# Kernel optimization log

Hardware: AMD Instinct MI355X
Metric: run time of the kernel (lower is better)

Reference implementation:

```python
import jax, jax.numpy as jnp
import numpy as np

PAD_IDX = 1
NEG_BIG = jnp.float32(-1e18)


def setup_inputs() -> dict:
    key = jax.random.key(0)
    ks = jax.random.split(key, 7)
    B, L, K, D, V, C = 64, 350, 8, 300, 50000, 20
    node_sets = jax.random.randint(ks[0], (B, L), 0, V, dtype=jnp.int64)
    embedded_node = jax.random.normal(ks[1], (B, L, D), dtype=jnp.float32)
    edge_weight = jax.random.uniform(ks[2], (B, L, K), dtype=jnp.float32)
    embedded_neighbor_node = jax.random.normal(ks[3], (B, L, K, D), dtype=jnp.float32)
    information_rate = jax.random.uniform(ks[4], (V, 1), dtype=jnp.float32)
    W = jax.random.normal(ks[5], (C, D), dtype=jnp.float32) * 0.05
    b = jax.random.normal(ks[6], (C,), dtype=jnp.float32) * 0.05
    return {"node_sets": node_sets, "embedded_node": embedded_node,
            "edge_weight": edge_weight,
            "embedded_neighbor_node": embedded_neighbor_node,
            "information_rate": information_rate, "W": W, "b": b}


def reference(node_sets, embedded_node, edge_weight, embedded_neighbor_node,
              information_rate, W, b):
    # weighted neighbor messages: [B,L,K,D]
    tmp = edge_weight[..., None] * embedded_neighbor_node
    # masked_fill(tmp == 0, -1e18); dropout_rate=0 -> identity
    tmp = jnp.where(tmp == 0, NEG_BIG, tmp)
    # max-pool over neighbors K -> [B,L,D]
    M = tmp.max(axis=2)
    # gather per-node information rate [B,L,1]; padding nodes forced to 1
    ir = information_rate[node_sets]
    ir = jnp.where((node_sets == PAD_IDX)[..., None], jnp.float32(1.0), ir)
    # gated combine, sum over nodes L -> [B,D]
    combined = (1.0 - ir) * M + ir * embedded_node
    s = combined.sum(axis=1)
    # linear + relu + softmax -> [B,C]
    x = jax.nn.relu(jnp.einsum('bd,cd->bc', s, W) + b)
    return jax.nn.softmax(x, axis=1)
```

## Files before the change

kernel.cpp:

```cpp
#include <hip/hip_runtime.h>
#include <math.h>

#define Bn 64
#define Ln 350
#define Kn 8
#define Dn 300
#define Cn 20
#define SPLIT 32
#define PAD_IDX 1
#define NEG_BIG (-1e18f)

__global__ __launch_bounds__(256) void mp_reduce(
    const int* __restrict__ node_sets,
    const float* __restrict__ emb_node,
    const float* __restrict__ edge_w,
    const float* __restrict__ emb_nbr,
    const float* __restrict__ info_rate,
    float* __restrict__ s_out)
{
    __shared__ __align__(16) float sAcc[4][Dn + 4];

    const int bid  = blockIdx.x;
    const int b    = bid / SPLIT;
    const int sidx = bid % SPLIT;
    const int tid  = threadIdx.x;
    const int wave = tid >> 6;
    const int lane = tid & 63;
    const bool has1 = (lane < (Dn / 4 - 64));

    float4 acc0 = make_float4(0.f, 0.f, 0.f, 0.f);
    float4 acc1 = make_float4(0.f, 0.f, 0.f, 0.f);

    for (int j = wave;; j += 4) {
        const int l = sidx + j * SPLIT;
        if (l >= Ln) break;
        const size_t row = (size_t)b * Ln + l;

        const float* ewp = edge_w + row * Kn;
        float ewv[Kn];
        #pragma unroll
        for (int k = 0; k < Kn; ++k) ewv[k] = ewp[k];

        const int node = node_sets[row];
        const float ir = (node == PAD_IDX) ? 1.0f : info_rate[node];
        const float om = 1.0f - ir;

        const float* nb = emb_nbr + row * (size_t)(Kn * Dn);
        const float* en = emb_node + row * (size_t)Dn;

        {
            float4 m = make_float4(NEG_BIG, NEG_BIG, NEG_BIG, NEG_BIG);
            #pragma unroll
            for (int k = 0; k < Kn; ++k) {
                const float4 v = *reinterpret_cast<const float4*>(nb + k * Dn + 4 * lane);
                const float w = ewv[k];
                float x0 = w * v.x, x1 = w * v.y, x2 = w * v.z, x3 = w * v.w;
                x0 = (x0 == 0.f) ? NEG_BIG : x0;
                x1 = (x1 == 0.f) ? NEG_BIG : x1;
                x2 = (x2 == 0.f) ? NEG_BIG : x2;
                x3 = (x3 == 0.f) ? NEG_BIG : x3;
                m.x = fmaxf(m.x, x0);
                m.y = fmaxf(m.y, x1);
                m.z = fmaxf(m.z, x2);
                m.w = fmaxf(m.w, x3);
            }
            const float4 e = *reinterpret_cast<const float4*>(en + 4 * lane);
            acc0.x += om * m.x + ir * e.x;
            acc0.y += om * m.y + ir * e.y;
            acc0.z += om * m.z + ir * e.z;
            acc0.w += om * m.w + ir * e.w;
        }

        if (has1) {
            const int off = 256 + 4 * lane;
            float4 m = make_float4(NEG_BIG, NEG_BIG, NEG_BIG, NEG_BIG);
            #pragma unroll
            for (int k = 0; k < Kn; ++k) {
                const float4 v = *reinterpret_cast<const float4*>(nb + k * Dn + off);
                const float w = ewv[k];
                float x0 = w * v.x, x1 = w * v.y, x2 = w * v.z, x3 = w * v.w;
                x0 = (x0 == 0.f) ? NEG_BIG : x0;
                x1 = (x1 == 0.f) ? NEG_BIG : x1;
                x2 = (x2 == 0.f) ? NEG_BIG : x2;
                x3 = (x3 == 0.f) ? NEG_BIG : x3;
                m.x = fmaxf(m.x, x0);
                m.y = fmaxf(m.y, x1);
                m.z = fmaxf(m.z, x2);
                m.w = fmaxf(m.w, x3);
            }
            const float4 e = *reinterpret_cast<const float4*>(en + off);
            acc1.x += om * m.x + ir * e.x;
            acc1.y += om * m.y + ir * e.y;
            acc1.z += om * m.z + ir * e.z;
            acc1.w += om * m.w + ir * e.w;
        }
    }

    *reinterpret_cast<float4*>(&sAcc[wave][4 * lane]) = acc0;
    if (has1) *reinterpret_cast<float4*>(&sAcc[wave][256 + 4 * lane]) = acc1;
    __syncthreads();

    for (int d = tid; d < Dn; d += 256) {
        const float sum = sAcc[0][d] + sAcc[1][d] + sAcc[2][d] + sAcc[3][d];
        atomicAdd(&s_out[b * Dn + d], sum);
    }
}

__global__ __launch_bounds__(64) void mp_head(
    const float* __restrict__ s_in,
    const float* __restrict__ Wm,
    const float* __restrict__ bias,
    float* __restrict__ out)
{
    __shared__ float ssh[Dn];
    __shared__ float xsh[Cn];

    const int b = blockIdx.x;
    const int t = threadIdx.x;

    for (int d = t; d < Dn; d += 64) ssh[d] = s_in[b * Dn + d];
    __syncthreads();

    if (t < Cn) {
        float acc = bias[t];
        const float* wr = Wm + t * Dn;
        for (int d = 0; d < Dn; ++d) acc += ssh[d] * wr[d];
        xsh[t] = fmaxf(acc, 0.f);
    }
    __syncthreads();

    if (t < Cn) {
        float mx = xsh[0];
        #pragma unroll
        for (int i = 1; i < Cn; ++i) mx = fmaxf(mx, xsh[i]);
        float sum = 0.f;
        #pragma unroll
        for (int i = 0; i < Cn; ++i) sum += expf(xsh[i] - mx);
        out[b * Cn + t] = expf(xsh[t] - mx) / sum;
    }
}

extern "C" void kernel_launch(void* const* d_in, const int* in_sizes, int n_in,
                              void* d_out, int out_size, void* d_ws, size_t ws_size,
                              hipStream_t stream) {
    const int*   node_sets = (const int*)d_in[0];
    const float* emb_node  = (const float*)d_in[1];
    const float* edge_w    = (const float*)d_in[2];
    const float* emb_nbr   = (const float*)d_in[3];
    const float* info_rate = (const float*)d_in[4];
    const float* Wm        = (const float*)d_in[5];
    const float* bias      = (const float*)d_in[6];
    float* out  = (float*)d_out;
    float* s_ws = (float*)d_ws;

    hipMemsetAsync(d_ws, 0, (size_t)Bn * Dn * sizeof(float), stream);

    mp_reduce<<<dim3(Bn * SPLIT), 256, 0, stream>>>(
        node_sets, emb_node, edge_w, emb_nbr, info_rate, s_ws);

    mp_head<<<dim3(Bn), 64, 0, stream>>>(s_ws, Wm, bias, out);
}
```

Baseline: 54.64 us.

## Write per-block partials instead of atomics, use nontemporal loads, vectorize edge weights

The reduce kernel now writes per-block partial sums into the workspace when it is large enough. The head kernel sums those SPLIT partials, which removes the memset launch and the global atomics. The large neighbor and node embedding loads use nontemporal loads to avoid polluting the cache, and the edge weights are loaded as two vector loads. The head's dot product is split across four accumulators. The cost is a larger workspace (Bn*SPLIT*Dn floats) and more serial summation work in the head kernel.

```diff
diff --git a/kernel.cpp b/kernel.cpp
--- a/kernel.cpp
+++ b/kernel.cpp
@@ -10,13 +10,20 @@
 #define PAD_IDX 1
 #define NEG_BIG (-1e18f)
 
+typedef float v4f __attribute__((ext_vector_type(4)));
+
+__device__ __forceinline__ v4f ntload4(const float* p) {
+    return __builtin_nontemporal_load(reinterpret_cast<const v4f*>(p));
+}
+
+template <bool PARTIAL>
 __global__ __launch_bounds__(256) void mp_reduce(
     const int* __restrict__ node_sets,
     const float* __restrict__ emb_node,
     const float* __restrict__ edge_w,
     const float* __restrict__ emb_nbr,
     const float* __restrict__ info_rate,
-    float* __restrict__ s_out)
+    float* __restrict__ ws)
 {
     __shared__ __align__(16) float sAcc[4][Dn + 4];
 
@@ -28,8 +35,8 @@
     const int lane = tid & 63;
     const bool has1 = (lane < (Dn / 4 - 64));
 
-    float4 acc0 = make_float4(0.f, 0.f, 0.f, 0.f);
-    float4 acc1 = make_float4(0.f, 0.f, 0.f, 0.f);
+    v4f acc0 = (v4f)(0.f);
+    v4f acc1 = (v4f)(0.f);
 
     for (int j = wave;; j += 4) {
         const int l = sidx + j * SPLIT;
@@ -37,9 +44,9 @@
         const size_t row = (size_t)b * Ln + l;
 
         const float* ewp = edge_w + row * Kn;
-        float ewv[Kn];
-        #pragma unroll
-        for (int k = 0; k < Kn; ++k) ewv[k] = ewp[k];
+        const v4f ew0 = *reinterpret_cast<const v4f*>(ewp);
+        const v4f ew1 = *reinterpret_cast<const v4f*>(ewp + 4);
+        float ewv[Kn] = {ew0.x, ew0.y, ew0.z, ew0.w, ew1.x, ew1.y, ew1.z, ew1.w};
 
         const int node = node_sets[row];
         const float ir = (node == PAD_IDX) ? 1.0f : info_rate[node];
@@ -49,10 +56,10 @@
         const float* en = emb_node + row * (size_t)Dn;
 
         {
-            float4 m = make_float4(NEG_BIG, NEG_BIG, NEG_BIG, NEG_BIG);
+            v4f m = (v4f)(NEG_BIG);
             #pragma unroll
             for (int k = 0; k < Kn; ++k) {
-                const float4 v = *reinterpret_cast<const float4*>(nb + k * Dn + 4 * lane);
+                const v4f v = ntload4(nb + k * Dn + 4 * lane);
                 const float w = ewv[k];
                 float x0 = w * v.x, x1 = w * v.y, x2 = w * v.z, x3 = w * v.w;
                 x0 = (x0 == 0.f) ? NEG_BIG : x0;
@@ -64,7 +71,7 @@
                 m.z = fmaxf(m.z, x2);
                 m.w = fmaxf(m.w, x3);
             }
-            const float4 e = *reinterpret_cast<const float4*>(en + 4 * lane);
+            const v4f e = ntload4(en + 4 * lane);
             acc0.x += om * m.x + ir * e.x;
             acc0.y += om * m.y + ir * e.y;
             acc0.z += om * m.z + ir * e.z;
@@ -73,10 +80,10 @@
 
         if (has1) {
             const int off = 256 + 4 * lane;
-            float4 m = make_float4(NEG_BIG, NEG_BIG, NEG_BIG, NEG_BIG);
+            v4f m = (v4f)(NEG_BIG);
             #pragma unroll
             for (int k = 0; k < Kn; ++k) {
-                const float4 v = *reinterpret_cast<const float4*>(nb + k * Dn + off);
+                const v4f v = ntload4(nb + k * Dn + off);
                 const float w = ewv[k];
                 float x0 = w * v.x, x1 = w * v.y, x2 = w * v.z, x3 = w * v.w;
                 x0 = (x0 == 0.f) ? NEG_BIG : x0;
@@ -88,7 +95,7 @@
                 m.z = fmaxf(m.z, x2);
                 m.w = fmaxf(m.w, x3);
             }
-            const float4 e = *reinterpret_cast<const float4*>(en + off);
+            const v4f e = ntload4(en + off);
             acc1.x += om * m.x + ir * e.x;
             acc1.y += om * m.y + ir * e.y;
             acc1.z += om * m.z + ir * e.z;
@@ -96,18 +103,25 @@
         }
     }
 
-    *reinterpret_cast<float4*>(&sAcc[wave][4 * lane]) = acc0;
-    if (has1) *reinterpret_cast<float4*>(&sAcc[wave][256 + 4 * lane]) = acc1;
+    *reinterpret_cast<v4f*>(&sAcc[wave][4 * lane]) = acc0;
+    if (has1) *reinterpret_cast<v4f*>(&sAcc[wave][256 + 4 * lane]) = acc1;
     __syncthreads();
 
-    for (int d = tid; d < Dn; d += 256) {
-        const float sum = sAcc[0][d] + sAcc[1][d] + sAcc[2][d] + sAcc[3][d];
-        atomicAdd(&s_out[b * Dn + d], sum);
+    if (PARTIAL) {
+        float* dst = ws + (size_t)bid * Dn;
+        for (int d = tid; d < Dn; d += 256)
+            dst[d] = sAcc[0][d] + sAcc[1][d] + sAcc[2][d] + sAcc[3][d];
+    } else {
+        for (int d = tid; d < Dn; d += 256) {
+            const float sum = sAcc[0][d] + sAcc[1][d] + sAcc[2][d] + sAcc[3][d];
+            atomicAdd(&ws[b * Dn + d], sum);
+        }
     }
 }
 
+template <int NPART>
 __global__ __launch_bounds__(64) void mp_head(
-    const float* __restrict__ s_in,
+    const float* __restrict__ part,
     const float* __restrict__ Wm,
     const float* __restrict__ bias,
     float* __restrict__ out)
@@ -118,14 +132,26 @@
     const int b = blockIdx.x;
     const int t = threadIdx.x;
 
-    for (int d = t; d < Dn; d += 64) ssh[d] = s_in[b * Dn + d];
+    for (int d = t; d < Dn; d += 64) {
+        const float* p = part + (size_t)b * NPART * Dn + d;
+        float s = 0.f;
+        #pragma unroll
+        for (int k = 0; k < NPART; ++k) s += p[k * Dn];
+        ssh[d] = s;
+    }
     __syncthreads();
 
     if (t < Cn) {
-        float acc = bias[t];
         const float* wr = Wm + t * Dn;
-        for (int d = 0; d < Dn; ++d) acc += ssh[d] * wr[d];
-        xsh[t] = fmaxf(acc, 0.f);
+        float a0 = 0.f, a1 = 0.f, a2 = 0.f, a3 = 0.f;
+        #pragma unroll 4
+        for (int d = 0; d < Dn; d += 4) {
+            a0 += ssh[d + 0] * wr[d + 0];
+            a1 += ssh[d + 1] * wr[d + 1];
+            a2 += ssh[d + 2] * wr[d + 2];
+            a3 += ssh[d + 3] * wr[d + 3];
+        }
+        xsh[t] = fmaxf(a0 + a1 + a2 + a3 + bias[t], 0.f);
     }
     __syncthreads();
 
@@ -151,12 +177,17 @@
     const float* Wm        = (const float*)d_in[5];
     const float* bias      = (const float*)d_in[6];
     float* out  = (float*)d_out;
-    float* s_ws = (float*)d_ws;
+    float* ws   = (float*)d_ws;
 
-    hipMemsetAsync(d_ws, 0, (size_t)Bn * Dn * sizeof(float), stream);
-
-    mp_reduce<<<dim3(Bn * SPLIT), 256, 0, stream>>>(
-        node_sets, emb_node, edge_w, emb_nbr, info_rate, s_ws);
-
-    mp_head<<<dim3(Bn), 64, 0, stream>>>(s_ws, Wm, bias, out);
+    const size_t need = (size_t)Bn * SPLIT * Dn * sizeof(float);
+    if (ws_size >= need) {
+        mp_reduce<true><<<dim3(Bn * SPLIT), 256, 0, stream>>>(
+            node_sets, emb_node, edge_w, emb_nbr, info_rate, ws);
+        mp_head<SPLIT><<<dim3(Bn), 64, 0, stream>>>(ws, Wm, bias, out);
+    } else {
+        hipMemsetAsync(d_ws, 0, (size_t)Bn * Dn * sizeof(float), stream);
+        mp_reduce<false><<<dim3(Bn * SPLIT), 256, 0, stream>>>(
+            node_sets, emb_node, edge_w, emb_nbr, info_rate, ws);
+        mp_head<1><<<dim3(Bn), 64, 0, stream>>>(ws, Wm, bias, out);
+    }
 }
```

New measurement: 58.34 us. 6.8% more time.
